# Optimization experiments

Hardware: AMD Instinct MI355X
Metric: run time of the kernel (lower is better)

The kernel has to match this reference:

```python
import jax, jax.numpy as jnp
import numpy as np

C = 256
NUM_HEADS = 4
HEAD_DIM = C // NUM_HEADS
GROUPS = 32
EPS = 1e-5


def setup_inputs() -> dict:
    key = jax.random.key(0)
    ks = jax.random.split(key, 7)
    B, H, W = 4, 64, 64
    x = jax.random.normal(ks[0], (B, C, H, W), dtype=jnp.float32)
    gn_w = jax.random.normal(ks[1], (C,), dtype=jnp.float32) * 0.02 + 1.0
    gn_b = jax.random.normal(ks[2], (C,), dtype=jnp.float32) * 0.02
    qkv_w = jax.random.normal(ks[3], (3 * C, C), dtype=jnp.float32) * (1.0 / np.sqrt(C))
    qkv_b = jax.random.normal(ks[4], (3 * C,), dtype=jnp.float32) * 0.02
    out_w = jax.random.normal(ks[5], (C, C), dtype=jnp.float32) * (1.0 / np.sqrt(C))
    out_b = jax.random.normal(ks[6], (C,), dtype=jnp.float32) * 0.02
    return {"x": x, "gn_w": gn_w, "gn_b": gn_b, "qkv_w": qkv_w,
            "qkv_b": qkv_b, "out_w": out_w, "out_b": out_b}


def _group_norm(x, w, b):
    # x: [B, C, H, W]; normalize over (C/GROUPS, H, W) per group
    B, Cc, Hh, Ww = x.shape
    xg = x.reshape(B, GROUPS, Cc // GROUPS, Hh, Ww)
    mean = jnp.mean(xg, axis=(2, 3, 4), keepdims=True)
    var = jnp.var(xg, axis=(2, 3, 4), keepdims=True)
    xg = (xg - mean) * jax.lax.rsqrt(var + EPS)
    xn = xg.reshape(B, Cc, Hh, Ww)
    return xn * w[None, :, None, None] + b[None, :, None, None]


def reference(x, gn_w, gn_b, qkv_w, qkv_b, out_w, out_b):
    B, Cc, Hh, Ww = x.shape
    N = Hh * Ww
    h = _group_norm(x, gn_w, gn_b).reshape(B, Cc, N)
    # qkv conv1d (kernel size 1) == pointwise linear over channel dim
    qkv = jnp.einsum('oc,bcn->bon', qkv_w, h) + qkv_b[None, :, None]
    q, k, v = jnp.split(qkv, 3, axis=1)
    q = q.reshape(B, NUM_HEADS, HEAD_DIM, N)
    k = k.reshape(B, NUM_HEADS, HEAD_DIM, N)
    v = v.reshape(B, NUM_HEADS, HEAD_DIM, N)
    scale = 1.0 / np.sqrt(HEAD_DIM)
    attn = jnp.einsum('bhdk,bhdl->bhkl', q, k) * scale  # [B, H, N, N]
    attn = jax.nn.softmax(attn, axis=-1)
    out = jnp.einsum('bhkl,bhdl->bhdk', attn, v)  # [B, H, D, N]
    out = out.reshape(B, Cc, N)
    out = jnp.einsum('oc,bcn->bon', out_w, out) + out_b[None, :, None]
    return x + out.reshape(B, Cc, Hh, Ww)
```

## Files before the change

kernel.cpp:

```cpp
#include <hip/hip_runtime.h>
#include <cstdint>

typedef __bf16 bf16_t;
typedef __bf16 bf16x4 __attribute__((ext_vector_type(4)));
typedef __bf16 bf16x8 __attribute__((ext_vector_type(8)));
typedef float f32x4 __attribute__((ext_vector_type(4)));
typedef float f32x16 __attribute__((ext_vector_type(16)));
typedef unsigned int u32x2 __attribute__((ext_vector_type(2)));
typedef unsigned int u32x4 __attribute__((ext_vector_type(4)));

#define B_ 4
#define C_ 256
#define N_ 4096
#define NH_ 4
#define HD_ 64

static __device__ __forceinline__ f32x4 mfma_bf16(bf16x8 a, bf16x8 b, f32x4 c) {
  return __builtin_amdgcn_mfma_f32_16x16x32_bf16(a, b, c, 0, 0, 0);
}

static __device__ __forceinline__ f32x16 mfma32(bf16x8 a, bf16x8 b, f32x16 c) {
  return __builtin_amdgcn_mfma_f32_32x32x16_bf16(a, b, c, 0, 0, 0);
}

static __device__ __forceinline__ void async16(const void* g, void* l) {
  __builtin_amdgcn_global_load_lds(
      (__attribute__((address_space(1))) void*)(uintptr_t)g,
      (__attribute__((address_space(3))) void*)(uint32_t)(uintptr_t)l,
      16, 0, 0);
}

static __device__ __forceinline__ float fexp2(float x) {
#if __has_builtin(__builtin_amdgcn_exp2f)
  return __builtin_amdgcn_exp2f(x);
#else
  return exp2f(x);
#endif
}

static __device__ __forceinline__ unsigned pack_bf16(float lo, float hi) {
  bf16x4 t;
  t[0] = (bf16_t)lo;
  t[1] = (bf16_t)hi;
  return *(unsigned*)&t;
}

__global__ __launch_bounds__(256) void k_gn_stats(const float* __restrict__ x,
                                                  const float* __restrict__ gn_w,
                                                  const float* __restrict__ gn_b,
                                                  float* __restrict__ gnscale,
                                                  float* __restrict__ gnshift) {
  const int bg = blockIdx.x;
  const int b = bg >> 5, g = bg & 31;
  const float4* p4 = (const float4*)(x + (size_t)(b * C_ + g * 8) * N_);
  float s = 0.f, ss = 0.f;
  for (int i = threadIdx.x; i < 8192; i += 256) {
    float4 v = p4[i];
    s += (v.x + v.y) + (v.z + v.w);
    ss += (v.x * v.x + v.y * v.y) + (v.z * v.z + v.w * v.w);
  }
  for (int off = 32; off > 0; off >>= 1) {
    s += __shfl_down(s, off);
    ss += __shfl_down(ss, off);
  }
  __shared__ float red_s[4], red_ss[4];
  const int wid = threadIdx.x >> 6, lane = threadIdx.x & 63;
  if (lane == 0) { red_s[wid] = s; red_ss[wid] = ss; }
  __syncthreads();
  if (threadIdx.x < 8) {
    float S = (red_s[0] + red_s[1]) + (red_s[2] + red_s[3]);
    float SS = (red_ss[0] + red_ss[1]) + (red_ss[2] + red_ss[3]);
    float mean = S * (1.f / 32768.f);
    float var = SS * (1.f / 32768.f) - mean * mean;
    float rstd = rsqrtf(var + 1e-5f);
    int c = g * 8 + threadIdx.x;
    float w = gn_w[c];
    gnscale[b * C_ + c] = w * rstd;
    gnshift[b * C_ + c] = gn_b[c] - mean * rstd * w;
  }
}

__global__ __launch_bounds__(256) void k_conv_w(const float* __restrict__ qkv_w,
                                                const float* __restrict__ out_w,
                                                bf16_t* __restrict__ w1,
                                                bf16_t* __restrict__ w2) {
  int i = blockIdx.x * 256 + threadIdx.x;
  if (i < 3 * C_ * C_) w1[i] = (bf16_t)qkv_w[i];
  else w2[i - 3 * C_ * C_] = (bf16_t)out_w[i - 3 * C_ * C_];
}

__global__ __launch_bounds__(256) void k_gn_apply(const float* __restrict__ x,
                                                  const float* __restrict__ gnscale,
                                                  const float* __restrict__ gnshift,
                                                  bf16_t* __restrict__ h) {
  __shared__ bf16_t T[32 * 258];
  const int t = threadIdx.x;
  const int tok0 = blockIdx.x * 32;
  const int b = tok0 >> 12;
  const int n0 = tok0 & (N_ - 1);
  const int nl = t & 31, cset = t >> 5;
  const float* xb = x + ((size_t)(b * C_ + cset * 32) << 12) + n0 + nl;
  const float* scp = gnscale + b * C_ + cset * 32;
  const float* shp = gnshift + b * C_ + cset * 32;
#pragma unroll
  for (int j = 0; j < 32; ++j) {
    float y = xb[(size_t)j << 12] * scp[j] + shp[j];
    T[nl * 258 + cset * 32 + j] = (bf16_t)y;
  }
  __syncthreads();
  const int c4 = t & 63;
#pragma unroll
  for (int p = 0; p < 8; ++p) {
    const int tokl = p * 4 + (t >> 6);
    const int idx = tokl * 258 + c4 * 4;
    uint2 v;
    v.x = *(const unsigned*)&T[idx];
    v.y = *(const unsigned*)&T[idx + 2];
    *(uint2*)(h + ((size_t)(tok0 + tokl) << 8) + c4 * 4) = v;
  }
}

__global__ __launch_bounds__(256) void k_gemm_qkv(const bf16_t* __restrict__ h,
                                                  const bf16_t* __restrict__ w1,
                                                  const float* __restrict__ qkv_b,
                                                  bf16_t* __restrict__ Qb,
                                                  bf16_t* __restrict__ Kb,
                                                  bf16_t* __restrict__ Vb) {
  __shared__ bf16_t As[128 * 32], Bs[128 * 32];
  const int tid = threadIdx.x, lane = tid & 63, wid = tid >> 6;
  const int g = lane >> 4, q = lane & 15;
  const int wm = wid >> 1, wn = wid & 1;
  const int m0 = blockIdx.x * 128;
  const int o0 = blockIdx.y * 128;
  f32x4 acc[4][4] = {};
  const int srow = lane >> 2, scol = (lane & 3) * 8;
  for (int kc = 0; kc < 8; ++kc) {
    const int k0 = kc * 32;
#pragma unroll
    for (int j = 0; j < 2; ++j) {
      const int chunk = wid + j * 4;
      async16(h + (size_t)(m0 + chunk * 16 + srow) * C_ + k0 + scol, &As[chunk * 512]);
      async16(w1 + (size_t)(o0 + chunk * 16 + srow) * C_ + k0 + scol, &Bs[chunk * 512]);
    }
    __syncthreads();
    bf16x8 a[4], bb[4];
#pragma unroll
    for (int t = 0; t < 4; ++t) {
      a[t] = *(const bf16x8*)&As[(wm * 64 + t * 16 + q) * 32 + g * 8];
      bb[t] = *(const bf16x8*)&Bs[(wn * 64 + t * 16 + q) * 32 + g * 8];
    }
#pragma unroll
    for (int mi = 0; mi < 4; ++mi)
#pragma unroll
      for (int ni = 0; ni < 4; ++ni)
        acc[mi][ni] = mfma_bf16(a[mi], bb[ni], acc[mi][ni]);
    __syncthreads();
  }
  const float QSCALE = 0.1803368801111244f;
#pragma unroll
  for (int ni = 0; ni < 4; ++ni) {
    const int o = o0 + wn * 64 + ni * 16 + q;
    const float bias = qkv_b[o];
    const int mat = o >> 8;
    const int c = o & 255, hh = c >> 6, d = c & 63;
#pragma unroll
    for (int mi = 0; mi < 4; ++mi) {
      const int tokb = m0 + wm * 64 + mi * 16 + g * 4;
      const int b = tokb >> 12, n = tokb & (N_ - 1);
      const size_t bh = (size_t)(b * NH_ + hh);
      f32x4 t = acc[mi][ni] + bias;
      if (mat == 0) {
#pragma unroll
        for (int r = 0; r < 4; ++r)
          Qb[(bh * N_ + n + r) * HD_ + d] = (bf16_t)(t[r] * QSCALE);
      } else if (mat == 1) {
#pragma unroll
        for (int r = 0; r < 4; ++r)
          Kb[(bh * N_ + n + r) * HD_ + d] = (bf16_t)t[r];
      } else {
        *(bf16x4*)(Vb + (bh * HD_ + d) * N_ + n) = __builtin_convertvector(t, bf16x4);
      }
    }
  }
}

__global__ __launch_bounds__(512, 4) void k_attn(const bf16_t* __restrict__ Qb,
                                                 const bf16_t* __restrict__ Kb,
                                                 const bf16_t* __restrict__ Vb,
                                                 bf16_t* __restrict__ op0,
                                                 bf16_t* __restrict__ op1,
                                                 bf16_t* __restrict__ op23,
                                                 float* __restrict__ lsum) {
  __shared__ __align__(16) bf16_t Ks[2][4096];
  __shared__ __align__(16) bf16_t Vs[2][4096];
  const int tid = threadIdx.x, lane = tid & 63, wid = tid >> 6;
  const int l31 = lane & 31, hi = lane >> 5;
  const int r7 = l31 & 7;
  const int rk = r7 ^ (l31 >> 3);
  int bid = blockIdx.x;
  bid = (bid & 7) * 128 + (bid >> 3);
  const int kh = bid & 3;
  const int qt = (bid >> 2) & 15;
  const int bh = bid >> 6;
  const int nq0 = qt * 256 + wid * 32;
  const int k00 = kh * (N_ / 4);
  const int NT = (N_ / 4) / 64;
  const size_t base = (size_t)bh << 18;
  const bf16_t* Qp = Qb + base;
  const bf16_t* Kp = Kb + base;
  const bf16_t* Vp = Vb + base;

  bf16x8 bq[4];
#pragma unroll
  for (int i = 0; i < 4; ++i)
    bq[i] = *(const bf16x8*)(Qp + (size_t)(nq0 + l31) * HD_ + i * 16 + hi * 8);

  const int srow = lane >> 3;
  const int sc16 = ((lane & 7) ^ srow ^ wid) & 7;

  f32x16 acc0 = {}, acc1 = {};
  float lacc = 0.f;

  async16(Kp + (size_t)(k00 + wid * 8 + srow) * HD_ + sc16 * 8, &Ks[0][wid * 512]);
  async16(Vp + (size_t)(wid * 8 + srow) * N_ + k00 + sc16 * 8, &Vs[0][wid * 512]);
  __syncthreads();

  const bf16_t* kS = Kp + (size_t)(k00 + 64 + wid * 8 + srow) * HD_ + sc16 * 8;
  const bf16_t* vS = Vp + (size_t)(wid * 8 + srow) * N_ + k00 + 64 + sc16 * 8;

  for (int t = 0; t < NT; ++t) {
    const int buf = t & 1;
    if (t < NT - 1) {
      async16(kS, &Ks[buf ^ 1][wid * 512]);
      async16(vS, &Vs[buf ^ 1][wid * 512]);
      kS += 64 * HD_;
      vS += 64;
    }
    const bf16_t* Kl = Ks[buf];
    const bf16_t* Vl = Vs[buf];
    f32x16 s0, s1;
    const f32x16 z = {};
    __builtin_amdgcn_s_setprio(1);
#pragma unroll
    for (int i = 0; i < 4; ++i) {
      bf16x8 k0 = *(const bf16x8*)(Kl + l31 * 64 + ((((2 * i + hi) ^ rk) & 7) * 8));
      bf16x8 k1 = *(const bf16x8*)(Kl + (32 + l31) * 64 + ((((2 * i + hi) ^ rk ^ 4) & 7) * 8));
      if (i == 0) {
        s0 = mfma32(k0, bq[0], z);
        s1 = mfma32(k1, bq[0], z);
      } else {
        s0 = mfma32(k0, bq[i], s0);
        s1 = mfma32(k1, bq[i], s1);
      }
    }
    __builtin_amdgcn_s_setprio(0);
#pragma unroll
    for (int r = 0; r < 16; ++r) {
      s0[r] = fexp2(s0[r]);
      s1[r] = fexp2(s1[r]);
    }
    float lt0 = 0.f, lt1 = 0.f;
#pragma unroll
    for (int r = 0; r < 16; ++r) {
      lt0 += s0[r];
      lt1 += s1[r];
    }
    lacc += lt0 + lt1;
    bf16x8 pb[4];
#pragma unroll
    for (int kc = 0; kc < 4; ++kc) {
      const int bs = (kc & 1) * 8;
      unsigned uA, uB, uC, uD;
      if (kc < 2) {
        uA = pack_bf16(s0[bs + 0], s0[bs + 1]);
        uB = pack_bf16(s0[bs + 2], s0[bs + 3]);
        uC = pack_bf16(s0[bs + 4], s0[bs + 5]);
        uD = pack_bf16(s0[bs + 6], s0[bs + 7]);
      } else {
        uA = pack_bf16(s1[bs + 0], s1[bs + 1]);
        uB = pack_bf16(s1[bs + 2], s1[bs + 3]);
        uC = pack_bf16(s1[bs + 4], s1[bs + 5]);
        uD = pack_bf16(s1[bs + 6], s1[bs + 7]);
      }
      u32x4 w;
#if __has_builtin(__builtin_amdgcn_permlane32_swap)
      u32x2 sAC = __builtin_amdgcn_permlane32_swap(uA, uC, false, false);
      u32x2 sBD = __builtin_amdgcn_permlane32_swap(uB, uD, false, false);
      w[0] = sAC[0]; w[1] = sBD[0]; w[2] = sAC[1]; w[3] = sBD[1];
#else
      w[0] = (hi == 0) ? uA : (unsigned)__shfl((int)uC, l31);
      w[1] = (hi == 0) ? uB : (unsigned)__shfl((int)uD, l31);
      w[2] = (hi == 0) ? (unsigned)__shfl((int)uA, l31 + 32) : uC;
      w[3] = (hi == 0) ? (unsigned)__shfl((int)uB, l31 + 32) : uD;
#endif
      pb[kc] = *(bf16x8*)&w;
    }
    __builtin_amdgcn_s_setprio(1);
#pragma unroll
    for (int kc = 0; kc < 4; ++kc) {
      bf16x8 v0 = *(const bf16x8*)(Vl + l31 * 64 + ((((2 * kc + hi) ^ rk) & 7) * 8));
      bf16x8 v1 = *(const bf16x8*)(Vl + (32 + l31) * 64 + ((((2 * kc + hi) ^ rk ^ 4) & 7) * 8));
      acc0 = mfma32(v0, pb[kc], acc0);
      acc1 = mfma32(v1, pb[kc], acc1);
    }
    __builtin_amdgcn_s_setprio(0);
    __syncthreads();
  }

  lacc += __shfl_xor(lacc, 32);

  bf16_t* Op;
  if (kh == 0) Op = op0 + (size_t)bh * N_ * HD_;
  else if (kh == 1) Op = op1 + (size_t)bh * N_ * HD_;
  else Op = op23 + (size_t)((kh - 2) * 16 + bh) * N_ * HD_;
  Op += (size_t)(nq0 + l31) * HD_;
#pragma unroll
  for (int dt = 0; dt < 2; ++dt) {
    const f32x16& a = dt ? acc1 : acc0;
#pragma unroll
    for (int qd = 0; qd < 4; ++qd) {
      bf16x4 r;
#pragma unroll
      for (int m = 0; m < 4; ++m) r[m] = (bf16_t)a[qd * 4 + m];
      *(bf16x4*)(Op + dt * 32 + qd * 8 + hi * 4) = r;
    }
  }
  if (hi == 0) lsum[(size_t)(kh * 16 + bh) * N_ + nq0 + l31] = lacc;
}

__global__ __launch_bounds__(256) void k_attn_combine(const bf16_t* __restrict__ op0,
                                                      const bf16_t* __restrict__ op1,
                                                      const bf16_t* __restrict__ op23,
                                                      const float* __restrict__ lsum,
                                                      bf16_t* __restrict__ att) {
  const int gid = blockIdx.x * 256 + threadIdx.x;
  const int d8 = gid & 7;
  const int q = (gid >> 3) & (N_ - 1);
  const int bh = gid >> 15;
  const size_t ro = ((size_t)bh * N_ + q) * HD_ + d8 * 8;
  const float l = lsum[(size_t)bh * N_ + q] + lsum[(size_t)(16 + bh) * N_ + q] +
                  lsum[(size_t)(32 + bh) * N_ + q] + lsum[(size_t)(48 + bh) * N_ + q];
  const float inv = 1.0f / l;
  const bf16x8 o0 = *(const bf16x8*)(op0 + ro);
  const bf16x8 o1 = *(const bf16x8*)(op1 + ro);
  const bf16x8 o2 = *(const bf16x8*)(op23 + ro);
  const bf16x8 o3 = *(const bf16x8*)(op23 + (size_t)16 * N_ * HD_ + ro);
  bf16x8 r;
#pragma unroll
  for (int j = 0; j < 8; ++j)
    r[j] = (bf16_t)((((float)o0[j] + (float)o1[j]) + ((float)o2[j] + (float)o3[j])) * inv);
  const int b = bh >> 2, hh = bh & 3;
  *(bf16x8*)(att + ((size_t)b * N_ + q) * C_ + hh * HD_ + d8 * 8) = r;
}

__global__ __launch_bounds__(256) void k_gemm_out(const bf16_t* __restrict__ att,
                                                  const bf16_t* __restrict__ w2,
                                                  const float* __restrict__ out_b,
                                                  const float* __restrict__ x,
                                                  float* __restrict__ out) {
  __shared__ bf16_t As[128 * 32], Bs[128 * 32];
  const int tid = threadIdx.x, lane = tid & 63, wid = tid >> 6;
  const int g = lane >> 4, q = lane & 15;
  const int wm = wid >> 1, wn = wid & 1;
  const int m0 = blockIdx.x * 128;
  const int o0 = blockIdx.y * 128;
  f32x4 acc[4][4] = {};
  const int srow = lane >> 2, scol = (lane & 3) * 8;
  for (int kc = 0; kc < 8; ++kc) {
    const int k0 = kc * 32;
#pragma unroll
    for (int j = 0; j < 2; ++j) {
      const int chunk = wid + j * 4;
      async16(att + (size_t)(m0 + chunk * 16 + srow) * C_ + k0 + scol, &As[chunk * 512]);
      async16(w2 + (size_t)(o0 + chunk * 16 + srow) * C_ + k0 + scol, &Bs[chunk * 512]);
    }
    __syncthreads();
    bf16x8 a[4], bb[4];
#pragma unroll
    for (int t = 0; t < 4; ++t) {
      a[t] = *(const bf16x8*)&As[(wm * 64 + t * 16 + q) * 32 + g * 8];
      bb[t] = *(const bf16x8*)&Bs[(wn * 64 + t * 16 + q) * 32 + g * 8];
    }
#pragma unroll
    for (int mi = 0; mi < 4; ++mi)
#pragma unroll
      for (int ni = 0; ni < 4; ++ni)
        acc[mi][ni] = mfma_bf16(a[mi], bb[ni], acc[mi][ni]);
    __syncthreads();
  }
#pragma unroll
  for (int ni = 0; ni < 4; ++ni) {
    const int o = o0 + wn * 64 + ni * 16 + q;
    const float bias = out_b[o];
#pragma unroll
    for (int mi = 0; mi < 4; ++mi) {
      const int tokb = m0 + wm * 64 + mi * 16 + g * 4;
      const int b = tokb >> 12, n = tokb & (N_ - 1);
      const size_t idx = ((size_t)(b * C_ + o) << 12) + n;
      const float4 xv = *(const float4*)(x + idx);
      f32x4 t = acc[mi][ni];
      float4 r = make_float4(t[0] + bias + xv.x, t[1] + bias + xv.y,
                             t[2] + bias + xv.z, t[3] + bias + xv.w);
      *(float4*)(out + idx) = r;
    }
  }
}

extern "C" void kernel_launch(void* const* d_in, const int* in_sizes, int n_in,
                              void* d_out, int out_size, void* d_ws, size_t ws_size,
                              hipStream_t stream) {
  (void)in_sizes; (void)n_in; (void)out_size; (void)ws_size;
  const float* x = (const float*)d_in[0];
  const float* gn_w = (const float*)d_in[1];
  const float* gn_b = (const float*)d_in[2];
  const float* qkv_w = (const float*)d_in[3];
  const float* qkv_b = (const float*)d_in[4];
  const float* out_w = (const float*)d_in[5];
  const float* out_b = (const float*)d_in[6];
  float* out = (float*)d_out;

  char* ws = (char*)d_ws;
  float* gnscale = (float*)ws;
  float* gnshift = gnscale + 1024;
  bf16_t* w1bf = (bf16_t*)(ws + 8192);
  bf16_t* w2bf = w1bf + 196608;
  bf16_t* hbuf = w2bf + 65536;
  bf16_t* Qb = hbuf + 4194304;
  bf16_t* Kb = Qb + 4194304;
  bf16_t* Vb = Kb + 4194304;
  bf16_t* op1 = Vb + 4194304;
  float* lsum = (float*)(op1 + 4194304);
  bf16_t* op23 = (bf16_t*)d_out;

  k_gn_stats<<<128, 256, 0, stream>>>(x, gn_w, gn_b, gnscale, gnshift);
  k_conv_w<<<1024, 256, 0, stream>>>(qkv_w, out_w, w1bf, w2bf);
  k_gn_apply<<<512, 256, 0, stream>>>(x, gnscale, gnshift, hbuf);
  k_gemm_qkv<<<dim3(128, 6), 256, 0, stream>>>(hbuf, w1bf, qkv_b, Qb, Kb, Vb);
  k_attn<<<1024, 512, 0, stream>>>(Qb, Kb, Vb, hbuf, op1, op23, lsum);
  k_attn_combine<<<2048, 256, 0, stream>>>(hbuf, op1, op23, lsum, Qb);
  k_gemm_out<<<dim3(128, 2), 256, 0, stream>>>(Qb, w2bf, out_b, x, out);
}
```

Baseline: 136.6 us.

## Software-pipeline QK^T of next tile against softmax/PV of current tile

Moves from double to triple buffering of the K/V tiles in shared memory and prefetches two tiles ahead. The QK^T MFMAs for tile t+1 are issued before the exp2/pack/PV work of tile t, so matrix-core work can overlap the exponentials and permutes. The s_setprio hints are removed. In exchange it holds extra score registers live under a 512-thread, 4-block launch bound, which risks spills or lower occupancy, and it uses more LDS per block.

```diff
diff --git a/kernel.cpp b/kernel.cpp
--- a/kernel.cpp
+++ b/kernel.cpp
@@ -191,8 +191,8 @@
                                                  bf16_t* __restrict__ op1,
                                                  bf16_t* __restrict__ op23,
                                                  float* __restrict__ lsum) {
-  __shared__ __align__(16) bf16_t Ks[2][4096];
-  __shared__ __align__(16) bf16_t Vs[2][4096];
+  __shared__ __align__(16) bf16_t Ks[3][4096];
+  __shared__ __align__(16) bf16_t Vs[3][4096];
   const int tid = threadIdx.x, lane = tid & 63, wid = tid >> 6;
   const int l31 = lane & 31, hi = lane >> 5;
   const int r7 = l31 & 7;
@@ -223,65 +223,69 @@
 
   async16(Kp + (size_t)(k00 + wid * 8 + srow) * HD_ + sc16 * 8, &Ks[0][wid * 512]);
   async16(Vp + (size_t)(wid * 8 + srow) * N_ + k00 + sc16 * 8, &Vs[0][wid * 512]);
+  async16(Kp + (size_t)(k00 + 64 + wid * 8 + srow) * HD_ + sc16 * 8, &Ks[1][wid * 512]);
+  async16(Vp + (size_t)(wid * 8 + srow) * N_ + k00 + 64 + sc16 * 8, &Vs[1][wid * 512]);
   __syncthreads();
 
-  const bf16_t* kS = Kp + (size_t)(k00 + 64 + wid * 8 + srow) * HD_ + sc16 * 8;
-  const bf16_t* vS = Vp + (size_t)(wid * 8 + srow) * N_ + k00 + 64 + sc16 * 8;
-
+  const bf16_t* kS = Kp + (size_t)(k00 + 128 + wid * 8 + srow) * HD_ + sc16 * 8;
+  const bf16_t* vS = Vp + (size_t)(wid * 8 + srow) * N_ + k00 + 128 + sc16 * 8;
+
+  const f32x16 z = {};
+  f32x16 scA, scB;
+  {
+    const bf16_t* Kl = Ks[0];
+#pragma unroll
+    for (int i = 0; i < 4; ++i) {
+      bf16x8 k0 = *(const bf16x8*)(Kl + l31 * 64 + ((((2 * i + hi) ^ rk) & 7) * 8));
+      scA = (i == 0) ? mfma32(k0, bq[0], z) : mfma32(k0, bq[i], scA);
+    }
+#pragma unroll
+    for (int i = 0; i < 4; ++i) {
+      bf16x8 k1 = *(const bf16x8*)(Kl + (32 + l31) * 64 + ((((2 * i + hi) ^ rk ^ 4) & 7) * 8));
+      scB = (i == 0) ? mfma32(k1, bq[0], z) : mfma32(k1, bq[i], scB);
+    }
+  }
+
+  int cur = 0, nxt = 1, stg = 2;
   for (int t = 0; t < NT; ++t) {
-    const int buf = t & 1;
-    if (t < NT - 1) {
-      async16(kS, &Ks[buf ^ 1][wid * 512]);
-      async16(vS, &Vs[buf ^ 1][wid * 512]);
+    if (t < NT - 2) {
+      async16(kS, &Ks[stg][wid * 512]);
+      async16(vS, &Vs[stg][wid * 512]);
       kS += 64 * HD_;
       vS += 64;
     }
-    const bf16_t* Kl = Ks[buf];
-    const bf16_t* Vl = Vs[buf];
-    f32x16 s0, s1;
-    const f32x16 z = {};
-    __builtin_amdgcn_s_setprio(1);
+    const bf16_t* Kl = Ks[nxt];
+    f32x16 snA, snB;
 #pragma unroll
     for (int i = 0; i < 4; ++i) {
       bf16x8 k0 = *(const bf16x8*)(Kl + l31 * 64 + ((((2 * i + hi) ^ rk) & 7) * 8));
+      snA = (i == 0) ? mfma32(k0, bq[0], z) : mfma32(k0, bq[i], snA);
+    }
+#pragma unroll
+    for (int i = 0; i < 4; ++i) {
       bf16x8 k1 = *(const bf16x8*)(Kl + (32 + l31) * 64 + ((((2 * i + hi) ^ rk ^ 4) & 7) * 8));
-      if (i == 0) {
-        s0 = mfma32(k0, bq[0], z);
-        s1 = mfma32(k1, bq[0], z);
-      } else {
-        s0 = mfma32(k0, bq[i], s0);
-        s1 = mfma32(k1, bq[i], s1);
-      }
-    }
-    __builtin_amdgcn_s_setprio(0);
+      snB = (i == 0) ? mfma32(k1, bq[0], z) : mfma32(k1, bq[i], snB);
+    }
+#pragma unroll
+    for (int r = 0; r < 16; ++r) scA[r] = fexp2(scA[r]);
+#pragma unroll
+    for (int r = 0; r < 16; ++r) scB[r] = fexp2(scB[r]);
+    float lt0 = 0.f, lt1 = 0.f;
 #pragma unroll
     for (int r = 0; r < 16; ++r) {
-      s0[r] = fexp2(s0[r]);
-      s1[r] = fexp2(s1[r]);
-    }
-    float lt0 = 0.f, lt1 = 0.f;
-#pragma unroll
-    for (int r = 0; r < 16; ++r) {
-      lt0 += s0[r];
-      lt1 += s1[r];
+      lt0 += scA[r];
+      lt1 += scB[r];
     }
     lacc += lt0 + lt1;
     bf16x8 pb[4];
 #pragma unroll
     for (int kc = 0; kc < 4; ++kc) {
       const int bs = (kc & 1) * 8;
-      unsigned uA, uB, uC, uD;
-      if (kc < 2) {
-        uA = pack_bf16(s0[bs + 0], s0[bs + 1]);
-        uB = pack_bf16(s0[bs + 2], s0[bs + 3]);
-        uC = pack_bf16(s0[bs + 4], s0[bs + 5]);
-        uD = pack_bf16(s0[bs + 6], s0[bs + 7]);
-      } else {
-        uA = pack_bf16(s1[bs + 0], s1[bs + 1]);
-        uB = pack_bf16(s1[bs + 2], s1[bs + 3]);
-        uC = pack_bf16(s1[bs + 4], s1[bs + 5]);
-        uD = pack_bf16(s1[bs + 6], s1[bs + 7]);
-      }
+      const f32x16& sv = (kc < 2) ? scA : scB;
+      unsigned uA = pack_bf16(sv[bs + 0], sv[bs + 1]);
+      unsigned uB = pack_bf16(sv[bs + 2], sv[bs + 3]);
+      unsigned uC = pack_bf16(sv[bs + 4], sv[bs + 5]);
+      unsigned uD = pack_bf16(sv[bs + 6], sv[bs + 7]);
       u32x4 w;
 #if __has_builtin(__builtin_amdgcn_permlane32_swap)
       u32x2 sAC = __builtin_amdgcn_permlane32_swap(uA, uC, false, false);
@@ -295,7 +299,7 @@
 #endif
       pb[kc] = *(bf16x8*)&w;
     }
-    __builtin_amdgcn_s_setprio(1);
+    const bf16_t* Vl = Vs[cur];
 #pragma unroll
     for (int kc = 0; kc < 4; ++kc) {
       bf16x8 v0 = *(const bf16x8*)(Vl + l31 * 64 + ((((2 * kc + hi) ^ rk) & 7) * 8));
@@ -303,7 +307,9 @@
       acc0 = mfma32(v0, pb[kc], acc0);
       acc1 = mfma32(v1, pb[kc], acc1);
     }
-    __builtin_amdgcn_s_setprio(0);
+    scA = snA;
+    scB = snB;
+    const int tmp = cur; cur = nxt; nxt = stg; stg = tmp;
     __syncthreads();
   }
 
```

New measurement: 149.8 us. 9.6% more time.
